# Kernel tuning notes

Measured on AMD Instinct MI355X. Metric: run time of the kernel, lower is better.

## Reference

```python
import jax, jax.numpy as jnp
import numpy as np


def _chamfer(array1, array2):
    # array1: [B, N, 3], array2: [B, M, 3]
    sq1 = jnp.sum(array1 * array1, axis=-1)            # [B, N]
    sq2 = jnp.sum(array2 * array2, axis=-1)            # [B, M]
    inner = jnp.einsum('bnd,bmd->bnm', array1, array2)  # [B, N, M]
    d = sq1[:, :, None] + sq2[:, None, :] - 2.0 * inner  # [B, N, M]
    d = jnp.maximum(d, 0.0)  # clamp tiny negatives from cancellation
    dist1 = jnp.min(d, axis=2)  # [B, N] nearest in array2 for each pt in array1
    dist2 = jnp.min(d, axis=1)  # [B, M] nearest in array1 for each pt in array2
    return dist1, dist2


def setup_inputs() -> dict:
    key = jax.random.key(0)
    k1, k2 = jax.random.split(key)
    B, N, M = 8, 4096, 4096
    array1 = jax.random.normal(k1, (B, N, 3), dtype=jnp.float32)
    array2 = jax.random.normal(k2, (B, M, 3), dtype=jnp.float32)
    return {"array1": array1, "array2": array2}


def reference(array1, array2):
    dist1, dist2 = _chamfer(array1, array2)
    return jnp.mean(dist1) + jnp.mean(dist2)
```

## Files before the change

### kernel.cpp

```cpp
#include <hip/hip_runtime.h>
#include <math.h>

#define BATCH   8
#define NPTS    4096
#define TOTAL   (BATCH * NPTS)
#define THREADS 256
#define P       8
#define TILE    (THREADS * P)
#define TILES   (TOTAL / TILE)
#define CHUNKS  32
#define CHUNK   (NPTS / CHUNKS)
#define NBLOCK  (2 * TILES * CHUNKS)

typedef float v2f __attribute__((ext_vector_type(2)));


__global__ __launch_bounds__(THREADS)
void chamfer_kernel(const float* __restrict__ a1, const float* __restrict__ a2,
                    unsigned* __restrict__ dist) {
    const int bid   = blockIdx.x;
    const int dir   = bid >> 9;
    const int r     = bid & 511;
    const int tile  = r >> 5;
    const int chunk = r & 31;
    const int batch = tile >> 1;

    const float* __restrict__ sraw = dir ? a2 : a1;
    const float* __restrict__ qraw = dir ? a1 : a2;

    __shared__ float4 lA[CHUNK / 2];
    __shared__ float4 lB[CHUNK / 2];
    if (threadIdx.x < CHUNK / 2) {
        const int j = threadIdx.x;
        const int p = batch * NPTS + chunk * CHUNK + 2 * j;
        const float* __restrict__ g = qraw + 3 * p;
        float x0 = g[0], y0 = g[1], z0 = g[2];
        float x1 = g[3], y1 = g[4], z1 = g[5];
        lA[j] = make_float4(-2.0f * x0, -2.0f * x1, -2.0f * y0, -2.0f * y1);
        lB[j] = make_float4(-2.0f * z0, -2.0f * z1,
                            fmaf(x0, x0, fmaf(y0, y0, z0 * z0)),
                            fmaf(x1, x1, fmaf(y1, y1, z1 * z1)));
    }

    v2f xd[P], yd[P], zd[P];
    float sq[P];
    #pragma unroll
    for (int k = 0; k < P; k++) {
        int si = tile * TILE + k * THREADS + threadIdx.x;
        float x = sraw[3 * si + 0];
        float y = sraw[3 * si + 1];
        float z = sraw[3 * si + 2];
        xd[k] = (v2f){x, x};
        yd[k] = (v2f){y, y};
        zd[k] = (v2f){z, z};
        sq[k] = fmaf(x, x, fmaf(y, y, z * z));
    }
    __syncthreads();

    float acc[P];
    #pragma unroll
    for (int k = 0; k < P; k++) acc[k] = __builtin_inff();

    #pragma unroll 4
    for (int j = 0; j < CHUNK / 2; j++) {
        float4 A  = lA[j];
        float4 Bv = lB[j];
        v2f ax = {A.x, A.y};
        v2f ay = {A.z, A.w};
        v2f az = {Bv.x, Bv.y};
        v2f aw = {Bv.z, Bv.w};
        #pragma unroll
        for (int k = 0; k < P; k++) {
            v2f d = __builtin_elementwise_fma(az, zd[k], aw);
            d = __builtin_elementwise_fma(ay, yd[k], d);
            d = __builtin_elementwise_fma(ax, xd[k], d);
            acc[k] = fminf(fminf(d.x, d.y), acc[k]);
        }
    }

    #pragma unroll
    for (int k = 0; k < P; k++) {
        int si = tile * TILE + k * THREADS + threadIdx.x;
        float dmin = fmaxf(acc[k] + sq[k], 0.0f);
        atomicMin(dist + dir * TOTAL + si, __float_as_uint(dmin));
    }
}

__global__ __launch_bounds__(1024)
void reduce_kernel(const float* __restrict__ dist, float* __restrict__ out) {
    const float4* __restrict__ dv = (const float4*)dist;
    float s = 0.0f;
    #pragma unroll
    for (int i = 0; i < (2 * TOTAL / 4) / 1024; i++) {
        float4 v = dv[i * 1024 + threadIdx.x];
        s += (v.x + v.y) + (v.z + v.w);
    }
    #pragma unroll
    for (int off = 32; off > 0; off >>= 1) s += __shfl_down(s, off, 64);
    __shared__ float wsum[16];
    if ((threadIdx.x & 63) == 0) wsum[threadIdx.x >> 6] = s;
    __syncthreads();
    if (threadIdx.x < 16) {
        float v = wsum[threadIdx.x];
        #pragma unroll
        for (int off = 8; off > 0; off >>= 1) v += __shfl_down(v, off, 16);
        if (threadIdx.x == 0) out[0] = v * (1.0f / (float)TOTAL);
    }
}

extern "C" void kernel_launch(void* const* d_in, const int* in_sizes, int n_in,
                              void* d_out, int out_size, void* d_ws, size_t ws_size,
                              hipStream_t stream) {
    const float* a1 = (const float*)d_in[0];
    const float* a2 = (const float*)d_in[1];
    float* out = (float*)d_out;

    unsigned* dist = (unsigned*)d_ws;

    hipMemsetAsync(dist, 0xFF, (size_t)2 * TOTAL * sizeof(unsigned), stream);
    chamfer_kernel<<<NBLOCK, THREADS, 0, stream>>>(a1, a2, dist);
    reduce_kernel<<<1, 1024, 0, stream>>>((const float*)dist, out);
}
```

Baseline: 81.77 us.

## Replace atomicMin with per-chunk partial minima and parallel two-stage reduction

Halves points per thread (P 8→4), doubling block count to 2048 and adding an occupancy hint. Instead of atomicMin into a shared distance array, each block writes its chunk's minima to a partial buffer [2][32][TOTAL]. A new many-block reduction takes the min over chunks and sums with atomicAdd into the output. This removes atomic contention and the single-block reduction, but adds about 8MB of partial writes and reads plus more LDS traffic per FMA.

```diff
diff --git a/kernel.cpp b/kernel.cpp
--- a/kernel.cpp
+++ b/kernel.cpp
@@ -5,7 +5,7 @@
 #define NPTS    4096
 #define TOTAL   (BATCH * NPTS)
 #define THREADS 256
-#define P       8
+#define P       4
 #define TILE    (THREADS * P)
 #define TILES   (TOTAL / TILE)
 #define CHUNKS  32
@@ -15,15 +15,15 @@
 typedef float v2f __attribute__((ext_vector_type(2)));
 
 
-__global__ __launch_bounds__(THREADS)
+__global__ __launch_bounds__(THREADS, 8)
 void chamfer_kernel(const float* __restrict__ a1, const float* __restrict__ a2,
-                    unsigned* __restrict__ dist) {
+                    float* __restrict__ partial) {
     const int bid   = blockIdx.x;
-    const int dir   = bid >> 9;
-    const int r     = bid & 511;
+    const int dir   = bid >> 10;
+    const int r     = bid & 1023;
     const int tile  = r >> 5;
     const int chunk = r & 31;
-    const int batch = tile >> 1;
+    const int batch = tile >> 2;
 
     const float* __restrict__ sraw = dir ? a2 : a1;
     const float* __restrict__ qraw = dir ? a1 : a2;
@@ -78,33 +78,33 @@
         }
     }
 
+    float* __restrict__ prow = partial + (size_t)(dir * CHUNKS + chunk) * TOTAL;
     #pragma unroll
     for (int k = 0; k < P; k++) {
         int si = tile * TILE + k * THREADS + threadIdx.x;
-        float dmin = fmaxf(acc[k] + sq[k], 0.0f);
-        atomicMin(dist + dir * TOTAL + si, __float_as_uint(dmin));
+        prow[si] = fmaxf(acc[k] + sq[k], 0.0f);
     }
 }
 
-__global__ __launch_bounds__(1024)
-void reduce_kernel(const float* __restrict__ dist, float* __restrict__ out) {
-    const float4* __restrict__ dv = (const float4*)dist;
-    float s = 0.0f;
+__global__ __launch_bounds__(THREADS)
+void reduce1_kernel(const float* __restrict__ partial, float* __restrict__ out) {
+    const int tid = blockIdx.x * THREADS + threadIdx.x;
+    const int dir = tid >> 15;
+    const int si  = tid & (TOTAL - 1);
+    const float* __restrict__ col = partial + (size_t)dir * CHUNKS * TOTAL + si;
+    float m = __builtin_inff();
     #pragma unroll
-    for (int i = 0; i < (2 * TOTAL / 4) / 1024; i++) {
-        float4 v = dv[i * 1024 + threadIdx.x];
-        s += (v.x + v.y) + (v.z + v.w);
-    }
+    for (int c = 0; c < CHUNKS; c += 2)
+        m = fminf(fminf(col[c * TOTAL], col[(c + 1) * TOTAL]), m);
+    float s = m;
     #pragma unroll
     for (int off = 32; off > 0; off >>= 1) s += __shfl_down(s, off, 64);
-    __shared__ float wsum[16];
+    __shared__ float wsum[4];
     if ((threadIdx.x & 63) == 0) wsum[threadIdx.x >> 6] = s;
     __syncthreads();
-    if (threadIdx.x < 16) {
-        float v = wsum[threadIdx.x];
-        #pragma unroll
-        for (int off = 8; off > 0; off >>= 1) v += __shfl_down(v, off, 16);
-        if (threadIdx.x == 0) out[0] = v * (1.0f / (float)TOTAL);
+    if (threadIdx.x == 0) {
+        float bsum = (wsum[0] + wsum[1]) + (wsum[2] + wsum[3]);
+        atomicAdd(out, bsum * (1.0f / (float)TOTAL));
     }
 }
 
@@ -115,9 +115,9 @@
     const float* a2 = (const float*)d_in[1];
     float* out = (float*)d_out;
 
-    unsigned* dist = (unsigned*)d_ws;
+    float* partial = (float*)d_ws;
 
-    hipMemsetAsync(dist, 0xFF, (size_t)2 * TOTAL * sizeof(unsigned), stream);
-    chamfer_kernel<<<NBLOCK, THREADS, 0, stream>>>(a1, a2, dist);
-    reduce_kernel<<<1, 1024, 0, stream>>>((const float*)dist, out);
+    hipMemsetAsync(out, 0, sizeof(float), stream);
+    chamfer_kernel<<<NBLOCK, THREADS, 0, stream>>>(a1, a2, partial);
+    reduce1_kernel<<<(2 * TOTAL) / THREADS, THREADS, 0, stream>>>(partial, out);
 }
```

New measurement: 88.41 us. +8.1%, slower.
